# Optimization experiments

Hardware: AMD Instinct MI355X
Metric: run time of the kernel (lower is better)

## Reference

```python
import jax, jax.numpy as jnp
import numpy as np

N = 4096
IN_C, HID_C, OUT_C = 128, 256, 128


def setup_inputs() -> dict:
    key = jax.random.key(0)
    ks = jax.random.split(key, 6)
    return {
        "x": jax.random.normal(ks[0], (N, IN_C), jnp.float32),
        "attn_tensor": jax.random.normal(ks[1], (1, 12, N, N), jnp.float32),
        "agg_w": jax.random.normal(ks[2], (12,), jnp.float32),
        "agg_b": jax.random.normal(ks[3], (1,), jnp.float32),
        "W1": jax.random.normal(ks[4], (IN_C, HID_C), jnp.float32) * (IN_C ** -0.5),
        "b1": jnp.zeros((HID_C,), jnp.float32),
        "W2": jax.random.normal(ks[5], (HID_C, OUT_C), jnp.float32) * (HID_C ** -0.5),
        "b2": jnp.zeros((OUT_C,), jnp.float32),
    }


def reference(x, attn_tensor, agg_w, agg_b, W1, b1, W2, b2):
    # 1x1 conv over 12 channels -> [B, N, N]
    agg = jnp.einsum("bcuv,c->buv", attn_tensor, agg_w) + agg_b[0]
    # per-batch 0.9 quantile (torch.quantile default linear interpolation)
    thresh = jnp.quantile(agg.reshape(agg.shape[0], -1), 0.9, axis=1)
    mask = agg[0] >= thresh[0]                      # [N, N] boolean adjacency
    n = mask.shape[0]
    # dense adjacency; add remaining self-loops (PyG gcn_norm fill_value=1)
    A = jnp.maximum(mask.astype(x.dtype), jnp.eye(n, dtype=x.dtype))
    deg = A.sum(axis=0)                             # in-degree at target (col) index
    s = jnp.where(deg > 0, jax.lax.rsqrt(deg), 0.0)  # D^{-1/2}, inf -> 0

    def gcn(h, W, b):
        h = h @ W                                    # linear transform (no bias)
        # out[v] = s[v] * sum_u A[u, v] * s[u] * h[u]  (source->target flow)
        return s[:, None] * (A.T @ (s[:, None] * h)) + b

    h = jax.nn.relu(gcn(x, W1, b1))
    return gcn(h, W2, b2)
```

## Files before the change

kernel.cpp:

```cpp
#include <hip/hip_runtime.h>
#include <stdint.h>

#define N_NODES 4096
#define NNN ((int64_t)N_NODES * (int64_t)N_NODES)
#define TOTAL4 (NNN / 4)
#define NC 12
#define K0_RANK 15099493u

#define SROWS 164
#define SSTRIDE 25
#define LO_RANK 601210u
#define HI_RANK 607929u

#define M_SHIST 0
#define M_CH1   4096
#define M_CH2   4352
#define M_HB    8448
#define M_DEG   8704
#define M_CNTS  12800
#define M_BLO   13824
#define M_BHI   13825
#define M_NBEL  13826
#define M_MXM   13827
#define M_SELX  13828
#define M_WORDS 14336

#define CHUNK_V 16384

typedef __attribute__((ext_vector_type(4))) _Float16 half4v;
typedef __attribute__((ext_vector_type(2))) _Float16 half2v;

static __device__ __forceinline__ uint32_t f2key(float f) {
    uint32_t x = __float_as_uint(f);
    return (x & 0x80000000u) ? ~x : (x | 0x80000000u);
}
static __device__ __forceinline__ float key2f(uint32_t k) {
    uint32_t x = (k & 0x80000000u) ? (k & 0x7FFFFFFFu) : ~k;
    return __uint_as_float(x);
}

static __device__ __forceinline__ void select_bin(const uint32_t* __restrict__ gh,
        int nb, uint32_t target, uint32_t* hl, uint32_t* sc, uint32_t* out) {
    int t = threadIdx.x;
    int per = nb >> 8;
    for (int i = t; i < nb; i += 256) hl[i] = gh[i];
    __syncthreads();
    uint32_t p = 0;
    for (int i = 0; i < per; ++i) p += hl[t * per + i];
    sc[t] = p;
    __syncthreads();
    for (int d = 1; d < 256; d <<= 1) {
        uint32_t v = (t >= d) ? sc[t - d] : 0u;
        __syncthreads();
        sc[t] += v;
        __syncthreads();
    }
    uint32_t excl = sc[t] - p;
    if (p > 0 && target >= excl && target < excl + p) {
        uint32_t cum = excl; int b = t * per;
        while (cum + hl[b] <= target) { cum += hl[b]; ++b; }
        out[0] = (uint32_t)b; out[1] = target - cum;
    }
    __syncthreads();
}

__global__ __launch_bounds__(256) void sample_kernel(const float* __restrict__ attn,
        const float* __restrict__ w, const float* __restrict__ bb,
        uint32_t* __restrict__ meta) {
    __shared__ uint32_t h[4096];
    for (int i = threadIdx.x; i < 4096; i += 256) h[i] = 0;
    float wr[NC];
#pragma unroll
    for (int c = 0; c < NC; ++c) wr[c] = w[c];
    float b0 = bb[0];
    __syncthreads();
    const float4* a4 = (const float4*)attn;
    for (int idx = blockIdx.x * 256 + threadIdx.x; idx < SROWS * 1024; idx += 256 * 256) {
        int r = idx >> 10;
        int64_t off = (int64_t)(r * SSTRIDE) * 1024 + (idx & 1023);
        float ax = b0, ay = b0, az = b0, aw = b0;
#pragma unroll
        for (int c = 0; c < NC; ++c) {
            float4 t = a4[(int64_t)c * TOTAL4 + off];
            ax += wr[c] * t.x; ay += wr[c] * t.y; az += wr[c] * t.z; aw += wr[c] * t.w;
        }
        atomicAdd(&h[f2key(ax) >> 20], 1u);
        atomicAdd(&h[f2key(ay) >> 20], 1u);
        atomicAdd(&h[f2key(az) >> 20], 1u);
        atomicAdd(&h[f2key(aw) >> 20], 1u);
    }
    __syncthreads();
    for (int i = threadIdx.x; i < 4096; i += 256) {
        uint32_t c = h[i];
        if (c) atomicAdd(&meta[M_SHIST + i], c);
    }
}

__global__ __launch_bounds__(256) void bracket_kernel(uint32_t* __restrict__ meta) {
    __shared__ uint32_t hl[4096];
    __shared__ uint32_t sc[256];
    __shared__ uint32_t res[2];
    select_bin(meta + M_SHIST, 4096, LO_RANK, hl, sc, res);
    if (threadIdx.x == 0) meta[M_BLO] = res[0];
    __syncthreads();
    select_bin(meta + M_SHIST, 4096, HI_RANK, hl, sc, res);
    if (threadIdx.x == 0) meta[M_BHI] = res[0];
}

__global__ __launch_bounds__(256) void aggmask_kernel(const float* __restrict__ attn,
        const float* __restrict__ w, const float* __restrict__ bb,
        uint32_t* __restrict__ meta, uint32_t* __restrict__ M,
        float* __restrict__ candV, uint32_t* __restrict__ candC) {
    __shared__ uint32_t mrow[512];
    __shared__ uint32_t candH[256];
    __shared__ uint32_t cnt, nbel;
    int t = threadIdx.x;
    for (int i = t; i < 256; i += 256) candH[i] = 0;
    if (t == 0) { cnt = 0; nbel = 0; }
    float wr[NC];
#pragma unroll
    for (int c = 0; c < NC; ++c) wr[c] = w[c];
    float b0 = bb[0];
    uint32_t blo = meta[M_BLO], bhi = meta[M_BHI];
    __syncthreads();
    const float4* a4 = (const float4*)attn;
    float*    regV = candV + (size_t)blockIdx.x * CHUNK_V;
    uint32_t* regC = candC + (size_t)blockIdx.x * CHUNK_V;
    int64_t base = (int64_t)blockIdx.x * 4096;
    int u0 = blockIdx.x * 4;
    uint32_t below_t = 0;
    for (int it = 0; it < 16; ++it) {
        int li = it * 256 + t;
        float ax = b0, ay = b0, az = b0, aw = b0;
#pragma unroll
        for (int c = 0; c < NC; ++c) {
            float4 v = a4[(int64_t)c * TOTAL4 + base + li];
            ax += wr[c] * v.x; ay += wr[c] * v.y; az += wr[c] * v.z; aw += wr[c] * v.w;
        }
        int u = u0 + (li >> 10);
        int vcol = (li & 1023) * 4;
        float vals[4] = {ax, ay, az, aw};
        uint32_t nib = 0;
#pragma unroll
        for (int j = 0; j < 4; ++j) {
            float val = vals[j];
            uint32_t k = f2key(val);
            uint32_t top = k >> 20;
            if ((top > bhi) || (u == vcol + j)) nib |= (1u << j);
            if (top < blo) ++below_t;
            else if (top <= bhi) {
                uint32_t p = atomicAdd(&cnt, 1u);
                regV[p] = val;
                regC[p] = ((uint32_t)u << 12) | (uint32_t)(vcol + j);
                atomicAdd(&candH[min(top - blo, 255u)], 1u);
            }
        }
        uint32_t wd = nib << ((t & 7) * 4);
        wd |= (uint32_t)__shfl_xor((int)wd, 1);
        wd |= (uint32_t)__shfl_xor((int)wd, 2);
        wd |= (uint32_t)__shfl_xor((int)wd, 4);
        if ((t & 7) == 0) mrow[li >> 3] = wd;
    }
    atomicAdd(&nbel, below_t);
    __syncthreads();
    uint32_t* Mdst = M + (size_t)blockIdx.x * 512;
    Mdst[t] = mrow[t];
    Mdst[t + 256] = mrow[t + 256];
    uint32_t c = candH[t];
    if (c) atomicAdd(&meta[M_CH1 + t], c);
    if (t == 0) {
        meta[M_CNTS + blockIdx.x] = cnt;
        if (nbel) atomicAdd(&meta[M_NBEL], nbel);
    }
}

__global__ __launch_bounds__(256) void cand1_kernel(const float* __restrict__ candV,
        uint32_t* __restrict__ meta) {
    __shared__ uint32_t hl[4096];
    __shared__ uint32_t sc[256];
    __shared__ uint32_t res[2];
    int t = threadIdx.x;
    uint32_t r = K0_RANK - meta[M_NBEL];
    uint32_t blo = meta[M_BLO];
    select_bin(meta + M_CH1, 256, r, hl, sc, res);
    uint32_t b1c = blo + res[0];
    uint32_t r1 = res[1];
    if (t == 0) { meta[M_SELX + 0] = b1c; meta[M_SELX + 1] = r1; }
    for (int i = t; i < 4096; i += 256) hl[i] = 0;
    __syncthreads();
    uint32_t n = meta[M_CNTS + blockIdx.x];
    const float* region = candV + (size_t)blockIdx.x * CHUNK_V;
    for (uint32_t i = t; i < n; i += 256) {
        uint32_t key = f2key(region[i]);
        if ((key >> 20) == b1c) atomicAdd(&hl[(key >> 8) & 0xFFFu], 1u);
    }
    __syncthreads();
    for (int i = t; i < 4096; i += 256) {
        uint32_t c = hl[i];
        if (c) atomicAdd(&meta[M_CH2 + i], c);
    }
}

__global__ __launch_bounds__(256) void cand2_kernel(const float* __restrict__ candV,
        uint32_t* __restrict__ meta) {
    __shared__ uint32_t hl[4096];
    __shared__ uint32_t sc[256];
    __shared__ uint32_t res[2];
    __shared__ uint32_t hB[256];
    __shared__ uint32_t ms;
    int t = threadIdx.x;
    uint32_t r1 = meta[M_SELX + 1];
    uint32_t b1c = meta[M_SELX + 0];
    select_bin(meta + M_CH2, 4096, r1, hl, sc, res);
    uint32_t p24 = (b1c << 12) | res[0];
    hB[t] = 0;
    if (t == 0) {
        ms = 0xFFFFFFFFu;
        meta[M_SELX + 2] = res[0]; meta[M_SELX + 3] = res[1];
    }
    uint32_t n = meta[M_CNTS + blockIdx.x];
    const float* region = candV + (size_t)blockIdx.x * CHUNK_V;
    __syncthreads();
    uint32_t mn = 0xFFFFFFFFu;
    for (uint32_t i = t; i < n; i += 256) {
        uint32_t key = f2key(region[i]);
        uint32_t hi = key >> 8;
        if (hi == p24) atomicAdd(&hB[key & 0xFFu], 1u);
        else if (hi > p24) mn = min(mn, key);
    }
    atomicMin(&ms, mn);
    __syncthreads();
    uint32_t c = hB[t];
    if (c) atomicAdd(&meta[M_HB + t], c);
    if (t == 0 && ms != 0xFFFFFFFFu) atomicMax(&meta[M_MXM], ~ms);
}

__global__ __launch_bounds__(256) void candfix_kernel(const float* __restrict__ candV,
        const uint32_t* __restrict__ candC, uint32_t* __restrict__ meta,
        uint32_t* __restrict__ M) {
    __shared__ uint32_t h[256];
    __shared__ float thr;
    int t = threadIdx.x;
    h[t] = meta[M_HB + t];
    __syncthreads();
    if (t == 0) {
        uint32_t b1c = meta[M_SELX + 0], b2c = meta[M_SELX + 2], r2 = meta[M_SELX + 3];
        uint32_t cum = 0; int b = 0;
        while (b < 255 && cum + h[b] <= r2) { cum += h[b]; ++b; }
        uint32_t key0 = (b1c << 20) | (b2c << 8) | (uint32_t)b;
        uint32_t cle = cum + h[b];
        uint32_t key1;
        if (cle >= r2 + 2u) key1 = key0;
        else {
            int nb = b + 1;
            while (nb < 256 && h[nb] == 0) ++nb;
            key1 = (nb < 256) ? ((b1c << 20) | (b2c << 8) | (uint32_t)nb) : ~meta[M_MXM];
        }
        float v0 = key2f(key0);
        float v1 = key2f(key1);
        thr = v0 + 0.5f * (v1 - v0);
        meta[M_SELX + 4] = __float_as_uint(thr);
    }
    __syncthreads();
    float th = thr;
    uint32_t n = meta[M_CNTS + blockIdx.x];
    const float*    regV = candV + (size_t)blockIdx.x * CHUNK_V;
    const uint32_t* regC = candC + (size_t)blockIdx.x * CHUNK_V;
    for (uint32_t i = t; i < n; i += 256) {
        if (regV[i] >= th) {
            uint32_t c = regC[i];
            uint32_t u = c >> 12, v = c & 0xFFFu;
            atomicOr(&M[(size_t)u * 128 + (v >> 5)], 1u << (v & 31u));
        }
    }
}

__global__ __launch_bounds__(256) void transposeB_kernel(const uint32_t* __restrict__ M,
        uint32_t* __restrict__ B, uint32_t* __restrict__ deg) {
    __shared__ uint32_t tile[4][64][2];
    int wave = threadIdx.x >> 6, lane = threadIdx.x & 63;
    int tileId = blockIdx.x * 4 + wave;
    int u0 = (tileId & 63) * 64;
    int v0 = (tileId >> 6) * 64;
    uint2 two = *(const uint2*)(M + (size_t)(u0 + lane) * 128 + (v0 >> 5));
    tile[wave][lane][0] = two.x;
    tile[wave][lane][1] = two.y;
    __syncthreads();
    int sh = lane & 31, hw = lane >> 5;
    uint32_t w0 = 0, w1 = 0;
#pragma unroll
    for (int i = 0; i < 32; ++i) {
        w0 |= ((tile[wave][i][hw] >> sh) & 1u) << i;
        w1 |= ((tile[wave][32 + i][hw] >> sh) & 1u) << i;
    }
    B[(size_t)(v0 + lane) * 128 + (u0 >> 5)]     = w0;
    B[(size_t)(v0 + lane) * 128 + (u0 >> 5) + 1] = w1;
    uint32_t d = __popc(w0) + __popc(w1);
    if (d) atomicAdd(&deg[v0 + lane], d);
}

__global__ __launch_bounds__(256) void gemm1_kernel(const float* __restrict__ x,
        const float* __restrict__ W1, const uint32_t* __restrict__ deg,
        _Float16* __restrict__ g) {
    __shared__ float xr[8 * 128];
    __shared__ float sr[8];
    int u0 = blockIdx.x * 8;
    int t = threadIdx.x;
    ((float4*)xr)[t] = ((const float4*)(x + (int64_t)u0 * 128))[t];
    if (t < 8) sr[t] = rsqrtf((float)deg[u0 + t]);
    __syncthreads();
    float acc[8] = {0, 0, 0, 0, 0, 0, 0, 0};
    for (int k = 0; k < 128; k += 4) {
        float w0 = W1[(k + 0) * 256 + t], w1 = W1[(k + 1) * 256 + t];
        float w2 = W1[(k + 2) * 256 + t], w3 = W1[(k + 3) * 256 + t];
#pragma unroll
        for (int r = 0; r < 8; ++r) {
            float4 xv = *(const float4*)&xr[r * 128 + k];
            acc[r] += xv.x * w0 + xv.y * w1 + xv.z * w2 + xv.w * w3;
        }
    }
#pragma unroll
    for (int r = 0; r < 8; ++r)
        g[(int64_t)(u0 + r) * 256 + t] = (_Float16)(sr[r] * acc[r]);
}

__global__ __launch_bounds__(256) void gemm2_kernel(const float* __restrict__ h1,
        const float* __restrict__ W2, const uint32_t* __restrict__ deg,
        _Float16* __restrict__ g2) {
    __shared__ float hr[8 * 256];
    __shared__ float sr[8];
    int u0 = blockIdx.x * 8;
    int t = threadIdx.x;
    const float4* h4 = (const float4*)(h1 + (int64_t)u0 * 256);
    ((float4*)hr)[t] = h4[t];
    ((float4*)hr)[t + 256] = h4[t + 256];
    if (t < 8) sr[t] = rsqrtf((float)deg[u0 + t]);
    __syncthreads();
    int col = t & 127;
    int roff = (t >> 7) * 4;
    float acc[4] = {0, 0, 0, 0};
    for (int k = 0; k < 256; k += 4) {
        float w0 = W2[(k + 0) * 128 + col], w1 = W2[(k + 1) * 128 + col];
        float w2 = W2[(k + 2) * 128 + col], w3 = W2[(k + 3) * 128 + col];
#pragma unroll
        for (int r = 0; r < 4; ++r) {
            float4 hv = *(const float4*)&hr[(roff + r) * 256 + k];
            acc[r] += hv.x * w0 + hv.y * w1 + hv.z * w2 + hv.w * w3;
        }
    }
#pragma unroll
    for (int r = 0; r < 4; ++r)
        g2[(int64_t)(u0 + roff + r) * 128 + col] = (_Float16)(sr[roff + r] * acc[r]);
}

static __device__ __forceinline__ uint32_t build_idx(const uint32_t* __restrict__ B,
                                                     int v, int t, uint16_t* idx) {
    const uint32_t* row = B + (int64_t)v * 128;
    uint32_t w0 = row[t], w1 = row[t + 64];
    uint32_t pc0 = __popc(w0), pc1 = __popc(w1);
    int s0 = (int)pc0, s1 = (int)pc1;
#pragma unroll
    for (int d = 1; d < 64; d <<= 1) {
        int a = __shfl_up(s0, d);
        int b = __shfl_up(s1, d);
        if (t >= d) { s0 += a; s1 += b; }
    }
    uint32_t tot0 = (uint32_t)__shfl(s0, 63);
    uint32_t cnt  = tot0 + (uint32_t)__shfl(s1, 63);
    uint32_t p = (uint32_t)s0 - pc0;
    uint32_t m = w0;
    int ub = t * 32;
    while (m) { int bi = __ffs(m) - 1; m &= m - 1; idx[p++] = (uint16_t)(ub + bi); }
    p = tot0 + (uint32_t)s1 - pc1;
    m = w1;
    ub = (t + 64) * 32;
    while (m) { int bi = __ffs(m) - 1; m &= m - 1; idx[p++] = (uint16_t)(ub + bi); }
    __syncthreads();
    return cnt;
}

__global__ __launch_bounds__(64) void spmm1_kernel(const uint32_t* __restrict__ B,
        const _Float16* __restrict__ g, const uint32_t* __restrict__ deg,
        const float* __restrict__ b1, float* __restrict__ h1) {
    __shared__ uint16_t idx[4096];
    int v = blockIdx.x;
    int t = threadIdx.x;
    uint32_t cnt = build_idx(B, v, t, idx);
    const half4v* g4 = (const half4v*)g;
    float4 acc = make_float4(0.f, 0.f, 0.f, 0.f);
    uint32_t i = 0;
    for (; i + 8 <= cnt; i += 8) {
#pragma unroll
        for (int q = 0; q < 8; ++q) {
            half4v a = g4[idx[i + q] * 64 + t];
            acc.x += (float)a[0]; acc.y += (float)a[1];
            acc.z += (float)a[2]; acc.w += (float)a[3];
        }
    }
    for (; i < cnt; ++i) {
        half4v a = g4[idx[i] * 64 + t];
        acc.x += (float)a[0]; acc.y += (float)a[1];
        acc.z += (float)a[2]; acc.w += (float)a[3];
    }
    float sv = rsqrtf((float)deg[v]);
    float4 bb = ((const float4*)b1)[t];
    float4 r;
    r.x = fmaxf(sv * acc.x + bb.x, 0.f);
    r.y = fmaxf(sv * acc.y + bb.y, 0.f);
    r.z = fmaxf(sv * acc.z + bb.z, 0.f);
    r.w = fmaxf(sv * acc.w + bb.w, 0.f);
    ((float4*)h1)[(int64_t)v * 64 + t] = r;
}

__global__ __launch_bounds__(64) void spmm2_kernel(const uint32_t* __restrict__ B,
        const _Float16* __restrict__ g2, const uint32_t* __restrict__ deg,
        const float* __restrict__ b2, float* __restrict__ out) {
    __shared__ uint16_t idx[4096];
    int v = blockIdx.x;
    int t = threadIdx.x;
    uint32_t cnt = build_idx(B, v, t, idx);
    const half2v* gp = (const half2v*)g2;
    float ax = 0.f, ay = 0.f;
    uint32_t i = 0;
    for (; i + 8 <= cnt; i += 8) {
#pragma unroll
        for (int q = 0; q < 8; ++q) {
            half2v a = gp[idx[i + q] * 64 + t];
            ax += (float)a[0]; ay += (float)a[1];
        }
    }
    for (; i < cnt; ++i) {
        half2v a = gp[idx[i] * 64 + t];
        ax += (float)a[0]; ay += (float)a[1];
    }
    float sv = rsqrtf((float)deg[v]);
    float2 bb = ((const float2*)b2)[t];
    float2 r;
    r.x = sv * ax + bb.x;
    r.y = sv * ay + bb.y;
    ((float2*)out)[(int64_t)v * 64 + t] = r;
}

extern "C" void kernel_launch(void* const* d_in, const int* in_sizes, int n_in,
                              void* d_out, int out_size, void* d_ws, size_t ws_size,
                              hipStream_t stream) {
    const float* x    = (const float*)d_in[0];
    const float* attn = (const float*)d_in[1];
    const float* aggw = (const float*)d_in[2];
    const float* aggb = (const float*)d_in[3];
    const float* W1   = (const float*)d_in[4];
    const float* b1   = (const float*)d_in[5];
    const float* W2   = (const float*)d_in[6];
    const float* b2   = (const float*)d_in[7];
    float* out = (float*)d_out;

    char* ws = (char*)d_ws;
    size_t OFF_META  = 0;
    size_t OFF_M     = OFF_META + 65536;
    size_t OFF_B     = OFF_M + (size_t)N_NODES * 128 * 4;
    size_t OFF_CV    = OFF_B + (size_t)N_NODES * 128 * 4;
    size_t OFF_CC    = OFF_CV + (size_t)1024 * CHUNK_V * 4;
    size_t OFF_G     = OFF_CC + (size_t)1024 * CHUNK_V * 4;
    size_t OFF_H1    = OFF_G + (size_t)N_NODES * 256 * 2;
    size_t OFF_G2    = OFF_H1 + (size_t)N_NODES * 256 * 4;

    uint32_t* meta  = (uint32_t*)(ws + OFF_META);
    uint32_t* Mm    = (uint32_t*)(ws + OFF_M);
    uint32_t* Bm    = (uint32_t*)(ws + OFF_B);
    float*    candV = (float*)(ws + OFF_CV);
    uint32_t* candC = (uint32_t*)(ws + OFF_CC);
    _Float16* g     = (_Float16*)(ws + OFF_G);
    float*    h1    = (float*)(ws + OFF_H1);
    _Float16* g2    = (_Float16*)(ws + OFF_G2);
    uint32_t* deg   = meta + M_DEG;

    hipMemsetAsync(meta, 0, (size_t)M_WORDS * 4, stream);

    sample_kernel<<<256, 256, 0, stream>>>(attn, aggw, aggb, meta);
    bracket_kernel<<<1, 256, 0, stream>>>(meta);
    aggmask_kernel<<<1024, 256, 0, stream>>>(attn, aggw, aggb, meta, Mm, candV, candC);
    cand1_kernel<<<1024, 256, 0, stream>>>(candV, meta);
    cand2_kernel<<<1024, 256, 0, stream>>>(candV, meta);
    candfix_kernel<<<1024, 256, 0, stream>>>(candV, candC, meta, Mm);
    transposeB_kernel<<<1024, 256, 0, stream>>>(Mm, Bm, deg);

    gemm1_kernel<<<512, 256, 0, stream>>>(x, W1, deg, g);
    spmm1_kernel<<<N_NODES, 64, 0, stream>>>(Bm, g, deg, b1, h1);
    gemm2_kernel<<<512, 256, 0, stream>>>(h1, W2, deg, g2);
    spmm2_kernel<<<N_NODES, 64, 0, stream>>>(Bm, g2, deg, b2, out);
}
```

Measured before the change: 366.4 us.

## Aggregate raw features before W1 and fuse both dense layers into one kernel

Uses associativity, computing A^T (s*x) on the 128-wide input instead of the 256-wide x@W1 product. The first sparse aggregation therefore gathers half as many channels. W1, bias, ReLU and W2 are then fused into one MLP kernel that keeps the hidden activations in shared memory, which removes a kernel launch and the h1 round trip. The fp16 conversion of x is folded into the sampling kernel. In exchange, each gathered neighbour now needs a per-neighbour deg load and rsqrt inside the inner loop, and x is rounded to fp16 before aggregation, which changes numerics slightly.

```diff
diff --git a/kernel.cpp b/kernel.cpp
--- a/kernel.cpp
+++ b/kernel.cpp
@@ -27,7 +27,6 @@
 
 #define CHUNK_V 16384
 
-typedef __attribute__((ext_vector_type(4))) _Float16 half4v;
 typedef __attribute__((ext_vector_type(2))) _Float16 half2v;
 
 static __device__ __forceinline__ uint32_t f2key(float f) {
@@ -66,7 +65,17 @@
 
 __global__ __launch_bounds__(256) void sample_kernel(const float* __restrict__ attn,
         const float* __restrict__ w, const float* __restrict__ bb,
-        uint32_t* __restrict__ meta) {
+        uint32_t* __restrict__ meta, const float* __restrict__ x,
+        _Float16* __restrict__ x_h) {
+    {
+        const float2* x2 = (const float2*)x;
+        half2v* xh2 = (half2v*)x_h;
+        for (int i = blockIdx.x * 256 + threadIdx.x; i < 262144; i += 256 * 256) {
+            float2 v = x2[i];
+            half2v h; h[0] = (_Float16)v.x; h[1] = (_Float16)v.y;
+            xh2[i] = h;
+        }
+    }
     __shared__ uint32_t h[4096];
     for (int i = threadIdx.x; i < 4096; i += 256) h[i] = 0;
     float wr[NC];
@@ -299,60 +308,6 @@
     if (d) atomicAdd(&deg[v0 + lane], d);
 }
 
-__global__ __launch_bounds__(256) void gemm1_kernel(const float* __restrict__ x,
-        const float* __restrict__ W1, const uint32_t* __restrict__ deg,
-        _Float16* __restrict__ g) {
-    __shared__ float xr[8 * 128];
-    __shared__ float sr[8];
-    int u0 = blockIdx.x * 8;
-    int t = threadIdx.x;
-    ((float4*)xr)[t] = ((const float4*)(x + (int64_t)u0 * 128))[t];
-    if (t < 8) sr[t] = rsqrtf((float)deg[u0 + t]);
-    __syncthreads();
-    float acc[8] = {0, 0, 0, 0, 0, 0, 0, 0};
-    for (int k = 0; k < 128; k += 4) {
-        float w0 = W1[(k + 0) * 256 + t], w1 = W1[(k + 1) * 256 + t];
-        float w2 = W1[(k + 2) * 256 + t], w3 = W1[(k + 3) * 256 + t];
-#pragma unroll
-        for (int r = 0; r < 8; ++r) {
-            float4 xv = *(const float4*)&xr[r * 128 + k];
-            acc[r] += xv.x * w0 + xv.y * w1 + xv.z * w2 + xv.w * w3;
-        }
-    }
-#pragma unroll
-    for (int r = 0; r < 8; ++r)
-        g[(int64_t)(u0 + r) * 256 + t] = (_Float16)(sr[r] * acc[r]);
-}
-
-__global__ __launch_bounds__(256) void gemm2_kernel(const float* __restrict__ h1,
-        const float* __restrict__ W2, const uint32_t* __restrict__ deg,
-        _Float16* __restrict__ g2) {
-    __shared__ float hr[8 * 256];
-    __shared__ float sr[8];
-    int u0 = blockIdx.x * 8;
-    int t = threadIdx.x;
-    const float4* h4 = (const float4*)(h1 + (int64_t)u0 * 256);
-    ((float4*)hr)[t] = h4[t];
-    ((float4*)hr)[t + 256] = h4[t + 256];
-    if (t < 8) sr[t] = rsqrtf((float)deg[u0 + t]);
-    __syncthreads();
-    int col = t & 127;
-    int roff = (t >> 7) * 4;
-    float acc[4] = {0, 0, 0, 0};
-    for (int k = 0; k < 256; k += 4) {
-        float w0 = W2[(k + 0) * 128 + col], w1 = W2[(k + 1) * 128 + col];
-        float w2 = W2[(k + 2) * 128 + col], w3 = W2[(k + 3) * 128 + col];
-#pragma unroll
-        for (int r = 0; r < 4; ++r) {
-            float4 hv = *(const float4*)&hr[(roff + r) * 256 + k];
-            acc[r] += hv.x * w0 + hv.y * w1 + hv.z * w2 + hv.w * w3;
-        }
-    }
-#pragma unroll
-    for (int r = 0; r < 4; ++r)
-        g2[(int64_t)(u0 + roff + r) * 128 + col] = (_Float16)(sr[roff + r] * acc[r]);
-}
-
 static __device__ __forceinline__ uint32_t build_idx(const uint32_t* __restrict__ B,
                                                      int v, int t, uint16_t* idx) {
     const uint32_t* row = B + (int64_t)v * 128;
@@ -379,37 +334,82 @@
     return cnt;
 }
 
-__global__ __launch_bounds__(64) void spmm1_kernel(const uint32_t* __restrict__ B,
-        const _Float16* __restrict__ g, const uint32_t* __restrict__ deg,
-        const float* __restrict__ b1, float* __restrict__ h1) {
+__global__ __launch_bounds__(64) void spmmX_kernel(const uint32_t* __restrict__ B,
+        const _Float16* __restrict__ x_h, const uint32_t* __restrict__ deg,
+        float* __restrict__ t_out) {
     __shared__ uint16_t idx[4096];
     int v = blockIdx.x;
     int t = threadIdx.x;
     uint32_t cnt = build_idx(B, v, t, idx);
-    const half4v* g4 = (const half4v*)g;
-    float4 acc = make_float4(0.f, 0.f, 0.f, 0.f);
+    const half2v* xp = (const half2v*)x_h;
+    float ax = 0.f, ay = 0.f;
     uint32_t i = 0;
     for (; i + 8 <= cnt; i += 8) {
 #pragma unroll
         for (int q = 0; q < 8; ++q) {
-            half4v a = g4[idx[i + q] * 64 + t];
-            acc.x += (float)a[0]; acc.y += (float)a[1];
-            acc.z += (float)a[2]; acc.w += (float)a[3];
+            int u = idx[i + q];
+            float su = rsqrtf((float)deg[u]);
+            half2v a = xp[u * 64 + t];
+            ax += su * (float)a[0]; ay += su * (float)a[1];
         }
     }
     for (; i < cnt; ++i) {
-        half4v a = g4[idx[i] * 64 + t];
-        acc.x += (float)a[0]; acc.y += (float)a[1];
-        acc.z += (float)a[2]; acc.w += (float)a[3];
+        int u = idx[i];
+        float su = rsqrtf((float)deg[u]);
+        half2v a = xp[u * 64 + t];
+        ax += su * (float)a[0]; ay += su * (float)a[1];
     }
     float sv = rsqrtf((float)deg[v]);
-    float4 bb = ((const float4*)b1)[t];
-    float4 r;
-    r.x = fmaxf(sv * acc.x + bb.x, 0.f);
-    r.y = fmaxf(sv * acc.y + bb.y, 0.f);
-    r.z = fmaxf(sv * acc.z + bb.z, 0.f);
-    r.w = fmaxf(sv * acc.w + bb.w, 0.f);
-    ((float4*)h1)[(int64_t)v * 64 + t] = r;
+    float2 r; r.x = sv * ax; r.y = sv * ay;
+    ((float2*)t_out)[(int64_t)v * 64 + t] = r;
+}
+
+__global__ __launch_bounds__(256) void mlp_kernel(const float* __restrict__ t_in,
+        const float* __restrict__ W1, const float* __restrict__ b1,
+        const float* __restrict__ W2, const uint32_t* __restrict__ deg,
+        _Float16* __restrict__ g2) {
+    __shared__ float tr[8 * 128];
+    __shared__ float h1s[8 * 256];
+    __shared__ float sr[8];
+    int u0 = blockIdx.x * 8;
+    int t = threadIdx.x;
+    ((float4*)tr)[t] = ((const float4*)(t_in + (int64_t)u0 * 128))[t];
+    if (t < 8) sr[t] = rsqrtf((float)deg[u0 + t]);
+    __syncthreads();
+    {
+        float acc[8] = {0, 0, 0, 0, 0, 0, 0, 0};
+        for (int k = 0; k < 128; k += 4) {
+            float w0 = W1[(k + 0) * 256 + t], w1 = W1[(k + 1) * 256 + t];
+            float w2 = W1[(k + 2) * 256 + t], w3 = W1[(k + 3) * 256 + t];
+#pragma unroll
+            for (int r = 0; r < 8; ++r) {
+                float4 tv = *(const float4*)&tr[r * 128 + k];
+                acc[r] += tv.x * w0 + tv.y * w1 + tv.z * w2 + tv.w * w3;
+            }
+        }
+        float bb = b1[t];
+#pragma unroll
+        for (int r = 0; r < 8; ++r)
+            h1s[r * 256 + t] = fmaxf(acc[r] + bb, 0.f);
+    }
+    __syncthreads();
+    {
+        int col = t & 127;
+        int roff = (t >> 7) * 4;
+        float acc[4] = {0, 0, 0, 0};
+        for (int k = 0; k < 256; k += 4) {
+            float w0 = W2[(k + 0) * 128 + col], w1 = W2[(k + 1) * 128 + col];
+            float w2 = W2[(k + 2) * 128 + col], w3 = W2[(k + 3) * 128 + col];
+#pragma unroll
+            for (int r = 0; r < 4; ++r) {
+                float4 hv = *(const float4*)&h1s[(roff + r) * 256 + k];
+                acc[r] += hv.x * w0 + hv.y * w1 + hv.z * w2 + hv.w * w3;
+            }
+        }
+#pragma unroll
+        for (int r = 0; r < 4; ++r)
+            g2[(int64_t)(u0 + roff + r) * 128 + col] = (_Float16)(sr[roff + r] * acc[r]);
+    }
 }
 
 __global__ __launch_bounds__(64) void spmm2_kernel(const uint32_t* __restrict__ B,
@@ -460,23 +460,23 @@
     size_t OFF_B     = OFF_M + (size_t)N_NODES * 128 * 4;
     size_t OFF_CV    = OFF_B + (size_t)N_NODES * 128 * 4;
     size_t OFF_CC    = OFF_CV + (size_t)1024 * CHUNK_V * 4;
-    size_t OFF_G     = OFF_CC + (size_t)1024 * CHUNK_V * 4;
-    size_t OFF_H1    = OFF_G + (size_t)N_NODES * 256 * 2;
-    size_t OFF_G2    = OFF_H1 + (size_t)N_NODES * 256 * 4;
+    size_t OFF_XH    = OFF_CC + (size_t)1024 * CHUNK_V * 4;
+    size_t OFF_T     = OFF_XH + (size_t)N_NODES * 128 * 2;
+    size_t OFF_G2    = OFF_T + (size_t)N_NODES * 128 * 4;
 
     uint32_t* meta  = (uint32_t*)(ws + OFF_META);
     uint32_t* Mm    = (uint32_t*)(ws + OFF_M);
     uint32_t* Bm    = (uint32_t*)(ws + OFF_B);
     float*    candV = (float*)(ws + OFF_CV);
     uint32_t* candC = (uint32_t*)(ws + OFF_CC);
-    _Float16* g     = (_Float16*)(ws + OFF_G);
-    float*    h1    = (float*)(ws + OFF_H1);
+    _Float16* x_h   = (_Float16*)(ws + OFF_XH);
+    float*    t_ws  = (float*)(ws + OFF_T);
     _Float16* g2    = (_Float16*)(ws + OFF_G2);
     uint32_t* deg   = meta + M_DEG;
 
     hipMemsetAsync(meta, 0, (size_t)M_WORDS * 4, stream);
 
-    sample_kernel<<<256, 256, 0, stream>>>(attn, aggw, aggb, meta);
+    sample_kernel<<<256, 256, 0, stream>>>(attn, aggw, aggb, meta, x, x_h);
     bracket_kernel<<<1, 256, 0, stream>>>(meta);
     aggmask_kernel<<<1024, 256, 0, stream>>>(attn, aggw, aggb, meta, Mm, candV, candC);
     cand1_kernel<<<1024, 256, 0, stream>>>(candV, meta);
@@ -484,8 +484,7 @@
     candfix_kernel<<<1024, 256, 0, stream>>>(candV, candC, meta, Mm);
     transposeB_kernel<<<1024, 256, 0, stream>>>(Mm, Bm, deg);
 
-    gemm1_kernel<<<512, 256, 0, stream>>>(x, W1, deg, g);
-    spmm1_kernel<<<N_NODES, 64, 0, stream>>>(Bm, g, deg, b1, h1);
-    gemm2_kernel<<<512, 256, 0, stream>>>(h1, W2, deg, g2);
+    spmmX_kernel<<<N_NODES, 64, 0, stream>>>(Bm, x_h, deg, t_ws);
+    mlp_kernel<<<512, 256, 0, stream>>>(t_ws, W1, b1, W2, deg, g2);
     spmm2_kernel<<<N_NODES, 64, 0, stream>>>(Bm, g2, deg, b2, out);
 }
```

Result: faster. 350.3 us (-4.4%).
